# Optimization experiments

Measured on AMD Instinct MI355X. Metric: run time of the kernel, lower is better.

Reference implementation:

```python
import jax, jax.numpy as jnp
import numpy as np

VOCAB = 50000
D = 256          # mem_emb_size == embedding_size (forced by o_q + u)
E = 256
H = E // 2       # LSTM hidden
HOPS = 3
N_MEM, MEM_WORDS = 2000, 50
BATCH, Q_LEN = 64, 50
N_CHOICE, CH_LEN = 4, 10


def setup_inputs() -> dict:
    key = jax.random.key(0)
    ks = jax.random.split(key, 12)
    emb_scale = 0.02
    proj_scale = 1.0 / np.sqrt(E)
    return {
        "memory": jax.random.randint(ks[0], (N_MEM, MEM_WORDS), 0, VOCAB),
        "ques": jax.random.randint(ks[1], (BATCH, Q_LEN), 0, VOCAB),
        "answerChoices": jax.random.randint(ks[2], (BATCH, N_CHOICE, CH_LEN), 0, VOCAB),
        "A_emb": jax.random.normal(ks[3], (HOPS, VOCAB, D), jnp.float32) * emb_scale,
        "B_emb": jax.random.normal(ks[4], (VOCAB, E), jnp.float32) * emb_scale,
        "C_emb": jax.random.normal(ks[5], (VOCAB, E), jnp.float32) * emb_scale,
        "U": jax.random.normal(ks[6], (D, E), jnp.float32) * proj_scale,
        "V": jax.random.normal(ks[7], (D, E), jnp.float32) * proj_scale,
        "W": jax.random.normal(ks[8], (D, D), jnp.float32) * proj_scale,
        "W_ih": jax.random.normal(ks[9], (4 * H, E), jnp.float32) * proj_scale,
        "W_hh": jax.random.normal(ks[10], (4 * H, H), jnp.float32) * (1.0 / np.sqrt(H)),
        "b_ih": jnp.zeros((4 * H,), jnp.float32),
        "b_hh": jnp.zeros((4 * H,), jnp.float32),
    }


def _lstm_final(x, W_ih, W_hh, b_ih, b_hh):
    # x: [B, T, E]; returns concat(h_T, c_T): [B, 2H] (torch gate order i,f,g,o)
    B = x.shape[0]
    Hh = W_hh.shape[1]
    b = b_ih + b_hh

    def step(carry, xt):
        h, c = carry
        g = xt @ W_ih.T + h @ W_hh.T + b
        i, f, gg, o = jnp.split(g, 4, axis=-1)
        c = jax.nn.sigmoid(f) * c + jax.nn.sigmoid(i) * jnp.tanh(gg)
        h = jax.nn.sigmoid(o) * jnp.tanh(c)
        return (h, c), None

    init = (jnp.zeros((B, Hh), x.dtype), jnp.zeros((B, Hh), x.dtype))
    (h, c), _ = jax.lax.scan(step, init, jnp.swapaxes(x, 0, 1))
    return jnp.concatenate([h, c], axis=-1)


def reference(memory, ques, answerChoices, A_emb, B_emb, C_emb, U, V, W,
              W_ih, W_hh, b_ih, b_hh):
    # question encoding: embed -> LSTM -> concat(h, c)   [B, E]
    u = _lstm_final(B_emb[ques], W_ih, W_hh, b_ih, b_hh)
    # answer choices: embedding-bag sum over words       [B, K, E]
    a = C_emb[answerChoices].sum(axis=2)

    hops = A_emb.shape[0]
    o_q = None
    o_a = None
    for hop in range(hops):
        # per-hop memory embedding (shared across batch): gather + sum  [N, D]
        M = A_emb[hop][memory].sum(axis=1)
        # question-side attention over memory slots
        p_q = jax.nn.softmax(jnp.einsum('nd,de,be->bn', M, U, u), axis=1)
        o_q = p_q @ M                      # [B, D]
        u = o_q + u
        # answer-side attention (all choices at once)
        p_a = jax.nn.softmax(jnp.einsum('nd,de,bke->bkn', M, V, a), axis=-1)
        o_a = jnp.einsum('bkn,nd->bkd', p_a, M)   # [B, K, D]
        a = o_a + a

    # prediction: o_q^T W o_a per choice  -> [B, K]
    pred = jnp.einsum('bd,dm,bkm->bk', o_q, W, o_a)
    return jax.nn.log_softmax(pred, axis=1)
```

## Files before the change

### kernel.cpp

```cpp
#include <hip/hip_runtime.h>
#include <hip/hip_bf16.h>
#include <math.h>

#define VOCAB 50000
#define DDIM 256
#define EDIM 256
#define HDIM 128
#define N_MEM 2000
#define MEM_WORDS 50
#define BATCH 64
#define Q_LEN 50
#define N_CHOICE 4
#define CH_LEN 10
#define NT 5
#define BT (BATCH * NT)

__device__ __forceinline__ float sigmoidf_(float x) {
    return 1.0f / (1.0f + expf(-x));
}

__global__ __launch_bounds__(256) void transpose_kernel(const float* __restrict__ in,
                                                        float* __restrict__ out,
                                                        int R, int C) {
    __shared__ float tile[32][33];
    int c0 = blockIdx.x * 32, r0 = blockIdx.y * 32;
    int tx = threadIdx.x & 31, ty = threadIdx.x >> 5;
    for (int i = ty; i < 32; i += 8) {
        int r = r0 + i, c = c0 + tx;
        tile[i][tx] = (r < R && c < C) ? in[(size_t)r * C + c] : 0.0f;
    }
    __syncthreads();
    for (int i = ty; i < 32; i += 8) {
        int r = c0 + i, c = r0 + tx;
        if (r < C && c < R) out[(size_t)r * R + c] = tile[tx][i];
    }
}

__global__ __launch_bounds__(256) void compute_M_kernel(const int* __restrict__ memory,
                                                        const float* __restrict__ A_emb,
                                                        float* __restrict__ M_all) {
    int n = blockIdx.x, hop = blockIdx.y, d = threadIdx.x;
    __shared__ int idx[MEM_WORDS];
    if (d < MEM_WORDS) idx[d] = memory[n * MEM_WORDS + d];
    __syncthreads();
    const float* base = A_emb + (size_t)hop * VOCAB * DDIM;
    float acc = 0.0f;
#pragma unroll 5
    for (int w = 0; w < MEM_WORDS; ++w) acc += base[(size_t)idx[w] * DDIM + d];
    M_all[((size_t)hop * N_MEM + n) * DDIM + d] = acc;
}

__global__ __launch_bounds__(256) void answer_bag_kernel(const int* __restrict__ ach,
                                                         const float* __restrict__ C_emb,
                                                         float* __restrict__ a) {
    int k = blockIdx.x, b = blockIdx.y, d = threadIdx.x;
    __shared__ int idx[CH_LEN];
    if (d < CH_LEN) idx[d] = ach[(b * N_CHOICE + k) * CH_LEN + d];
    __syncthreads();
    float acc = 0.0f;
#pragma unroll
    for (int w = 0; w < CH_LEN; ++w) acc += C_emb[(size_t)idx[w] * EDIM + d];
    a[(size_t)(b * N_CHOICE + k) * EDIM + d] = acc;
}

template <bool GATHER, bool BIAS>
__global__ __launch_bounds__(256) void gemm_abT_kernel(
    const float* __restrict__ A, const float* __restrict__ B, float* __restrict__ C,
    int M, int N, int K, const int* __restrict__ gidx,
    const float* __restrict__ bias1, const float* __restrict__ bias2) {
    __shared__ float As[16][64];
    __shared__ float Bs[16][64];
    __shared__ int rows[64];
    const int tid = threadIdx.x;
    const int m0 = blockIdx.x * 64;
    const int n0 = blockIdx.y * 64;
    const int lrow = tid >> 2;
    const int lk = (tid & 3) << 2;
    const int tx = tid & 15;
    const int ty = tid >> 4;
    if (GATHER) {
        if (tid < 64) rows[tid] = gidx[m0 + tid];
        __syncthreads();
    }
    float acc[4][4] = {};
    for (int k0 = 0; k0 < K; k0 += 16) {
        const float* ap = GATHER ? (A + (size_t)rows[lrow] * K)
                                 : (A + (size_t)(m0 + lrow) * K);
        float4 av = *(const float4*)(ap + k0 + lk);
        float4 bv = make_float4(0.f, 0.f, 0.f, 0.f);
        int brow = n0 + lrow;
        if (brow < N) bv = *(const float4*)(B + (size_t)brow * K + k0 + lk);
        __syncthreads();
        As[lk + 0][lrow] = av.x; As[lk + 1][lrow] = av.y;
        As[lk + 2][lrow] = av.z; As[lk + 3][lrow] = av.w;
        Bs[lk + 0][lrow] = bv.x; Bs[lk + 1][lrow] = bv.y;
        Bs[lk + 2][lrow] = bv.z; Bs[lk + 3][lrow] = bv.w;
        __syncthreads();
#pragma unroll
        for (int kk = 0; kk < 16; ++kk) {
            float4 a4 = *(const float4*)&As[kk][ty * 4];
            float4 b4 = *(const float4*)&Bs[kk][tx * 4];
            acc[0][0] += a4.x * b4.x; acc[0][1] += a4.x * b4.y; acc[0][2] += a4.x * b4.z; acc[0][3] += a4.x * b4.w;
            acc[1][0] += a4.y * b4.x; acc[1][1] += a4.y * b4.y; acc[1][2] += a4.y * b4.z; acc[1][3] += a4.y * b4.w;
            acc[2][0] += a4.z * b4.x; acc[2][1] += a4.z * b4.y; acc[2][2] += a4.z * b4.z; acc[2][3] += a4.z * b4.w;
            acc[3][0] += a4.w * b4.x; acc[3][1] += a4.w * b4.y; acc[3][2] += a4.w * b4.z; acc[3][3] += a4.w * b4.w;
        }
    }
#pragma unroll
    for (int i = 0; i < 4; ++i) {
        int m = m0 + ty * 4 + i;
#pragma unroll
        for (int j = 0; j < 4; ++j) {
            int n = n0 + tx * 4 + j;
            if (n < N) {
                float v = acc[i][j];
                if (BIAS) v += bias1[n] + bias2[n];
                C[(size_t)m * N + n] = v;
            }
        }
    }
}

__global__ __launch_bounds__(256) void gemm_ab_splitk_kernel(
    const float* __restrict__ A, const float* __restrict__ B, float* __restrict__ Cpart,
    int M, int N, int K, int KC) {
    __shared__ float As[16][64];
    __shared__ float Bs[16][64];
    const int tid = threadIdx.x;
    const int m0 = blockIdx.x * 64;
    const int n0 = blockIdx.y * 64;
    const int kstart = blockIdx.z * KC;
    const int kend = min(K, kstart + KC);
    const int arow = tid >> 2;
    const int alk = (tid & 3) << 2;
    const int bk = tid >> 4;
    const int bn = (tid & 15) << 2;
    const int tx = tid & 15;
    const int ty = tid >> 4;
    float acc[4][4] = {};
    for (int k0 = kstart; k0 < kend; k0 += 16) {
        float4 av = *(const float4*)(A + (size_t)(m0 + arow) * K + k0 + alk);
        float4 bv = *(const float4*)(B + (size_t)(k0 + bk) * N + n0 + bn);
        __syncthreads();
        As[alk + 0][arow] = av.x; As[alk + 1][arow] = av.y;
        As[alk + 2][arow] = av.z; As[alk + 3][arow] = av.w;
        *(float4*)&Bs[bk][bn] = bv;
        __syncthreads();
#pragma unroll
        for (int kk = 0; kk < 16; ++kk) {
            float4 a4 = *(const float4*)&As[kk][ty * 4];
            float4 b4 = *(const float4*)&Bs[kk][tx * 4];
            acc[0][0] += a4.x * b4.x; acc[0][1] += a4.x * b4.y; acc[0][2] += a4.x * b4.z; acc[0][3] += a4.x * b4.w;
            acc[1][0] += a4.y * b4.x; acc[1][1] += a4.y * b4.y; acc[1][2] += a4.y * b4.z; acc[1][3] += a4.y * b4.w;
            acc[2][0] += a4.z * b4.x; acc[2][1] += a4.z * b4.y; acc[2][2] += a4.z * b4.z; acc[2][3] += a4.z * b4.w;
            acc[3][0] += a4.w * b4.x; acc[3][1] += a4.w * b4.y; acc[3][2] += a4.w * b4.z; acc[3][3] += a4.w * b4.w;
        }
    }
    float* Cz = Cpart + (size_t)blockIdx.z * M * N;
#pragma unroll
    for (int i = 0; i < 4; ++i)
#pragma unroll
        for (int j = 0; j < 4; ++j)
            Cz[(size_t)(m0 + ty * 4 + i) * N + n0 + tx * 4 + j] = acc[i][j];
}

__global__ __launch_bounds__(512, 2) void lstm_kernel(const float* __restrict__ G0,
                                                      const float* __restrict__ WhhT,
                                                      float* __restrict__ u) {
    const int b = blockIdx.x;
    const int j = threadIdx.x;
    float w[HDIM];
#pragma unroll
    for (int h = 0; h < HDIM; ++h) w[h] = WhhT[(size_t)h * (4 * HDIM) + j];
    __shared__ float sh[HDIM];
    __shared__ float sg[4 * HDIM];
    float c = 0.0f;
    if (j < HDIM) sh[j] = 0.0f;
    __syncthreads();
    const float* g0p = G0 + (size_t)b * Q_LEN * (4 * HDIM) + j;
    for (int t = 0; t < Q_LEN; ++t) {
        float a0 = g0p[(size_t)t * (4 * HDIM)], a1 = 0.f, a2 = 0.f, a3 = 0.f;
#pragma unroll
        for (int h = 0; h < HDIM; h += 4) {
            float4 hv = *(const float4*)&sh[h];
            a0 += w[h + 0] * hv.x;
            a1 += w[h + 1] * hv.y;
            a2 += w[h + 2] * hv.z;
            a3 += w[h + 3] * hv.w;
        }
        sg[j] = (a0 + a1) + (a2 + a3);
        __syncthreads();
        if (j < HDIM) {
            float gi = sg[j], gf = sg[HDIM + j], gg = sg[2 * HDIM + j], go = sg[3 * HDIM + j];
            c = sigmoidf_(gf) * c + sigmoidf_(gi) * tanhf(gg);
            sh[j] = sigmoidf_(go) * tanhf(c);
        }
        __syncthreads();
    }
    if (j < HDIM) {
        u[(size_t)b * EDIM + j] = sh[j];
        u[(size_t)b * EDIM + HDIM + j] = c;
    }
}

__global__ __launch_bounds__(256) void proj_T_kernel(const float* __restrict__ u,
                                                     const float* __restrict__ a,
                                                     const float* __restrict__ UT,
                                                     const float* __restrict__ VT,
                                                     float* __restrict__ T) {
    const int tgt = blockIdx.x;
    const int b = blockIdx.y;
    const int d = threadIdx.x;
    __shared__ float sx[EDIM];
    const float* src = (tgt == 0) ? (u + (size_t)b * EDIM)
                                  : (a + (size_t)(b * N_CHOICE + tgt - 1) * EDIM);
    sx[d] = src[d];
    __syncthreads();
    const float* Wt = (tgt == 0) ? UT : VT;
    float acc = 0.0f;
#pragma unroll 4
    for (int e = 0; e < EDIM; ++e) acc += Wt[(size_t)e * DDIM + d] * sx[e];
    T[(size_t)(b * NT + tgt) * DDIM + d] = acc;
}

__global__ __launch_bounds__(256) void softmax_rows_kernel(float* __restrict__ S, int N) {
    const int row = blockIdx.x;
    float* x = S + (size_t)row * N;
    __shared__ float red[256];
    const int tid = threadIdx.x;
    float mx = -INFINITY;
    for (int i = tid; i < N; i += 256) mx = fmaxf(mx, x[i]);
    red[tid] = mx;
    __syncthreads();
    for (int s = 128; s > 0; s >>= 1) {
        if (tid < s) red[tid] = fmaxf(red[tid], red[tid + s]);
        __syncthreads();
    }
    mx = red[0];
    __syncthreads();
    float sum = 0.0f;
    for (int i = tid; i < N; i += 256) {
        float e = expf(x[i] - mx);
        x[i] = e;
        sum += e;
    }
    red[tid] = sum;
    __syncthreads();
    for (int s = 128; s > 0; s >>= 1) {
        if (tid < s) red[tid] += red[tid + s];
        __syncthreads();
    }
    float inv = 1.0f / red[0];
    for (int i = tid; i < N; i += 256) x[i] *= inv;
}

__global__ __launch_bounds__(256) void reduce_update_kernel(const float* __restrict__ Opart,
                                                            float* __restrict__ O,
                                                            float* __restrict__ u,
                                                            float* __restrict__ a) {
    const int bt = blockIdx.x;
    const int d = threadIdx.x;
    const size_t idx = (size_t)bt * DDIM + d;
    const size_t stride = (size_t)BT * DDIM;
    float v = Opart[idx] + Opart[stride + idx] + Opart[2 * stride + idx] + Opart[3 * stride + idx];
    O[idx] = v;
    const int b = bt / NT, t = bt % NT;
    if (t == 0) u[(size_t)b * EDIM + d] += v;
    else a[(size_t)(b * N_CHOICE + t - 1) * EDIM + d] += v;
}

__global__ __launch_bounds__(256) void predict_kernel(const float* __restrict__ O,
                                                      const float* __restrict__ W,
                                                      float* __restrict__ out) {
    const int b = blockIdx.x;
    const int m = threadIdx.x;
    __shared__ float soq[DDIM];
    __shared__ float red[256];
    __shared__ float scv[N_CHOICE];
    soq[m] = O[(size_t)(b * NT) * DDIM + m];
    __syncthreads();
    float wq = 0.0f;
#pragma unroll 4
    for (int d = 0; d < DDIM; ++d) wq += W[(size_t)d * DDIM + m] * soq[d];
    for (int k = 0; k < N_CHOICE; ++k) {
        red[m] = wq * O[(size_t)(b * NT + 1 + k) * DDIM + m];
        __syncthreads();
        for (int s = 128; s > 0; s >>= 1) {
            if (m < s) red[m] += red[m + s];
            __syncthreads();
        }
        if (m == 0) scv[k] = red[0];
        __syncthreads();
    }
    if (m == 0) {
        float mx = fmaxf(fmaxf(scv[0], scv[1]), fmaxf(scv[2], scv[3]));
        float s = 0.0f;
        for (int k = 0; k < N_CHOICE; ++k) s += expf(scv[k] - mx);
        float ls = mx + logf(s);
        for (int k = 0; k < N_CHOICE; ++k) out[b * N_CHOICE + k] = scv[k] - ls;
    }
}

extern "C" void kernel_launch(void* const* d_in, const int* in_sizes, int n_in,
                              void* d_out, int out_size, void* d_ws, size_t ws_size,
                              hipStream_t stream) {
    const int* memory = (const int*)d_in[0];
    const int* ques = (const int*)d_in[1];
    const int* ach = (const int*)d_in[2];
    const float* A_emb = (const float*)d_in[3];
    const float* B_emb = (const float*)d_in[4];
    const float* C_emb = (const float*)d_in[5];
    const float* U = (const float*)d_in[6];
    const float* V = (const float*)d_in[7];
    const float* W = (const float*)d_in[8];
    const float* W_ih = (const float*)d_in[9];
    const float* W_hh = (const float*)d_in[10];
    const float* b_ih = (const float*)d_in[11];
    const float* b_hh = (const float*)d_in[12];
    float* out = (float*)d_out;

    float* ws = (float*)d_ws;
    float* M_all = ws;
    float* G0 = M_all + 3 * N_MEM * DDIM;
    float* u = G0 + (size_t)BATCH * Q_LEN * 4 * HDIM;
    float* a = u + BATCH * EDIM;
    float* UT = a + BATCH * N_CHOICE * EDIM;
    float* VT = UT + EDIM * DDIM;
    float* WhhT = VT + EDIM * DDIM;
    float* T = G0;
    float* S = T + BT * DDIM;
    float* Opart = S + (size_t)BT * N_MEM;
    float* O = Opart + 4 * (size_t)BT * DDIM;

    transpose_kernel<<<dim3(8, 8), 256, 0, stream>>>(U, UT, DDIM, EDIM);
    transpose_kernel<<<dim3(8, 8), 256, 0, stream>>>(V, VT, DDIM, EDIM);
    transpose_kernel<<<dim3(4, 16), 256, 0, stream>>>(W_hh, WhhT, 4 * HDIM, HDIM);

    compute_M_kernel<<<dim3(N_MEM, 3), 256, 0, stream>>>(memory, A_emb, M_all);

    gemm_abT_kernel<true, true><<<dim3(50, 8), 256, 0, stream>>>(
        B_emb, W_ih, G0, BATCH * Q_LEN, 4 * HDIM, EDIM, ques, b_ih, b_hh);

    lstm_kernel<<<BATCH, 512, 0, stream>>>(G0, WhhT, u);

    answer_bag_kernel<<<dim3(N_CHOICE, BATCH), 256, 0, stream>>>(ach, C_emb, a);

    for (int hop = 0; hop < 3; ++hop) {
        const float* Mh = M_all + (size_t)hop * N_MEM * DDIM;
        proj_T_kernel<<<dim3(NT, BATCH), 256, 0, stream>>>(u, a, UT, VT, T);
        gemm_abT_kernel<false, false><<<dim3(5, 32), 256, 0, stream>>>(
            T, Mh, S, BT, N_MEM, DDIM, nullptr, nullptr, nullptr);
        softmax_rows_kernel<<<BT, 256, 0, stream>>>(S, N_MEM);
        gemm_ab_splitk_kernel<<<dim3(5, 4, 4), 256, 0, stream>>>(
            S, Mh, Opart, BT, DDIM, N_MEM, 512);
        reduce_update_kernel<<<BT, 256, 0, stream>>>(Opart, O, u, a);
    }

    predict_kernel<<<BATCH, 256, 0, stream>>>(O, W, out);
}
```

Before: 654.5 us.

## Vectorize memory gather, shrink GEMM tiles, deepen split-K, defer softmax normalization

The memory-embedding gather now reads float4 values, with four memory slots per block. The GEMM kernels switch to 32x64 tiles with 128 threads, which doubles the block count to better fill the GPU. The split-K for the attention-weighted sum goes from 4 to 10 chunks. Softmax normalization moves into the reduce step: it divides by the row sums there, saving one pass over S. In exchange there are more partial buffers to reduce and the extra workspace layout for the sums must be right.

```diff
diff --git a/kernel.cpp b/kernel.cpp
--- a/kernel.cpp
+++ b/kernel.cpp
@@ -14,6 +14,8 @@
 #define CH_LEN 10
 #define NT 5
 #define BT (BATCH * NT)
+#define OZ 10
+#define OKC 208
 
 __device__ __forceinline__ float sigmoidf_(float x) {
     return 1.0f / (1.0f + expf(-x));
@@ -39,15 +41,22 @@
 __global__ __launch_bounds__(256) void compute_M_kernel(const int* __restrict__ memory,
                                                         const float* __restrict__ A_emb,
                                                         float* __restrict__ M_all) {
-    int n = blockIdx.x, hop = blockIdx.y, d = threadIdx.x;
-    __shared__ int idx[MEM_WORDS];
-    if (d < MEM_WORDS) idx[d] = memory[n * MEM_WORDS + d];
-    __syncthreads();
-    const float* base = A_emb + (size_t)hop * VOCAB * DDIM;
-    float acc = 0.0f;
-#pragma unroll 5
-    for (int w = 0; w < MEM_WORDS; ++w) acc += base[(size_t)idx[w] * DDIM + d];
-    M_all[((size_t)hop * N_MEM + n) * DDIM + d] = acc;
+    const int hop = blockIdx.y;
+    const int tid = threadIdx.x;
+    const int slot = tid >> 6;
+    const int lane = tid & 63;
+    const int n = blockIdx.x * 4 + slot;
+    __shared__ int sidx[4 * MEM_WORDS];
+    if (tid < 4 * MEM_WORDS) sidx[tid] = memory[blockIdx.x * 4 * MEM_WORDS + tid];
+    __syncthreads();
+    const float* base = A_emb + (size_t)hop * VOCAB * DDIM + (lane << 2);
+    float4 acc = make_float4(0.f, 0.f, 0.f, 0.f);
+#pragma unroll 10
+    for (int w = 0; w < MEM_WORDS; ++w) {
+        float4 v = *(const float4*)(base + (size_t)sidx[slot * MEM_WORDS + w] * DDIM);
+        acc.x += v.x; acc.y += v.y; acc.z += v.z; acc.w += v.w;
+    }
+    *(float4*)&M_all[((size_t)hop * N_MEM + n) * DDIM + (lane << 2)] = acc;
 }
 
 __global__ __launch_bounds__(256) void answer_bag_kernel(const int* __restrict__ ach,
@@ -64,37 +73,41 @@
 }
 
 template <bool GATHER, bool BIAS>
-__global__ __launch_bounds__(256) void gemm_abT_kernel(
+__global__ __launch_bounds__(128) void gemm32_abT_kernel(
     const float* __restrict__ A, const float* __restrict__ B, float* __restrict__ C,
     int M, int N, int K, const int* __restrict__ gidx,
     const float* __restrict__ bias1, const float* __restrict__ bias2) {
-    __shared__ float As[16][64];
-    __shared__ float Bs[16][64];
-    __shared__ int rows[64];
+    __shared__ float As[16][36];
+    __shared__ float Bs[16][68];
+    __shared__ int rows[32];
     const int tid = threadIdx.x;
-    const int m0 = blockIdx.x * 64;
+    const int m0 = blockIdx.x * 32;
     const int n0 = blockIdx.y * 64;
-    const int lrow = tid >> 2;
-    const int lk = (tid & 3) << 2;
+    const int arow = tid >> 2;
+    const int ak4 = (tid & 3) << 2;
     const int tx = tid & 15;
     const int ty = tid >> 4;
     if (GATHER) {
-        if (tid < 64) rows[tid] = gidx[m0 + tid];
+        if (tid < 32) rows[tid] = gidx[m0 + tid];
         __syncthreads();
     }
     float acc[4][4] = {};
     for (int k0 = 0; k0 < K; k0 += 16) {
-        const float* ap = GATHER ? (A + (size_t)rows[lrow] * K)
-                                 : (A + (size_t)(m0 + lrow) * K);
-        float4 av = *(const float4*)(ap + k0 + lk);
-        float4 bv = make_float4(0.f, 0.f, 0.f, 0.f);
-        int brow = n0 + lrow;
-        if (brow < N) bv = *(const float4*)(B + (size_t)brow * K + k0 + lk);
-        __syncthreads();
-        As[lk + 0][lrow] = av.x; As[lk + 1][lrow] = av.y;
-        As[lk + 2][lrow] = av.z; As[lk + 3][lrow] = av.w;
-        Bs[lk + 0][lrow] = bv.x; Bs[lk + 1][lrow] = bv.y;
-        Bs[lk + 2][lrow] = bv.z; Bs[lk + 3][lrow] = bv.w;
+        const float* ap = GATHER ? (A + (size_t)rows[arow] * K)
+                                 : (A + (size_t)(m0 + arow) * K);
+        float4 av = *(const float4*)(ap + k0 + ak4);
+        float4 bv0 = make_float4(0.f, 0.f, 0.f, 0.f);
+        float4 bv1 = make_float4(0.f, 0.f, 0.f, 0.f);
+        int br0 = n0 + arow, br1 = n0 + 32 + arow;
+        if (br0 < N) bv0 = *(const float4*)(B + (size_t)br0 * K + k0 + ak4);
+        if (br1 < N) bv1 = *(const float4*)(B + (size_t)br1 * K + k0 + ak4);
+        __syncthreads();
+        As[ak4 + 0][arow] = av.x; As[ak4 + 1][arow] = av.y;
+        As[ak4 + 2][arow] = av.z; As[ak4 + 3][arow] = av.w;
+        Bs[ak4 + 0][arow] = bv0.x; Bs[ak4 + 1][arow] = bv0.y;
+        Bs[ak4 + 2][arow] = bv0.z; Bs[ak4 + 3][arow] = bv0.w;
+        Bs[ak4 + 0][32 + arow] = bv1.x; Bs[ak4 + 1][32 + arow] = bv1.y;
+        Bs[ak4 + 2][32 + arow] = bv1.z; Bs[ak4 + 3][32 + arow] = bv1.w;
         __syncthreads();
 #pragma unroll
         for (int kk = 0; kk < 16; ++kk) {
@@ -121,30 +134,32 @@
     }
 }
 
-__global__ __launch_bounds__(256) void gemm_ab_splitk_kernel(
+__global__ __launch_bounds__(128) void gemm32_ab_splitk_kernel(
     const float* __restrict__ A, const float* __restrict__ B, float* __restrict__ Cpart,
     int M, int N, int K, int KC) {
-    __shared__ float As[16][64];
-    __shared__ float Bs[16][64];
+    __shared__ float As[16][36];
+    __shared__ float Bs[16][68];
     const int tid = threadIdx.x;
-    const int m0 = blockIdx.x * 64;
+    const int m0 = blockIdx.x * 32;
     const int n0 = blockIdx.y * 64;
     const int kstart = blockIdx.z * KC;
     const int kend = min(K, kstart + KC);
     const int arow = tid >> 2;
-    const int alk = (tid & 3) << 2;
+    const int ak4 = (tid & 3) << 2;
     const int bk = tid >> 4;
     const int bn = (tid & 15) << 2;
     const int tx = tid & 15;
     const int ty = tid >> 4;
     float acc[4][4] = {};
     for (int k0 = kstart; k0 < kend; k0 += 16) {
-        float4 av = *(const float4*)(A + (size_t)(m0 + arow) * K + k0 + alk);
-        float4 bv = *(const float4*)(B + (size_t)(k0 + bk) * N + n0 + bn);
-        __syncthreads();
-        As[alk + 0][arow] = av.x; As[alk + 1][arow] = av.y;
-        As[alk + 2][arow] = av.z; As[alk + 3][arow] = av.w;
-        *(float4*)&Bs[bk][bn] = bv;
+        float4 av = *(const float4*)(A + (size_t)(m0 + arow) * K + k0 + ak4);
+        float4 bv0 = *(const float4*)(B + (size_t)(k0 + bk) * N + n0 + bn);
+        float4 bv1 = *(const float4*)(B + (size_t)(k0 + bk + 8) * N + n0 + bn);
+        __syncthreads();
+        As[ak4 + 0][arow] = av.x; As[ak4 + 1][arow] = av.y;
+        As[ak4 + 2][arow] = av.z; As[ak4 + 3][arow] = av.w;
+        *(float4*)&Bs[bk][bn] = bv0;
+        *(float4*)&Bs[bk + 8][bn] = bv1;
         __syncthreads();
 #pragma unroll
         for (int kk = 0; kk < 16; ++kk) {
@@ -223,7 +238,8 @@
     T[(size_t)(b * NT + tgt) * DDIM + d] = acc;
 }
 
-__global__ __launch_bounds__(256) void softmax_rows_kernel(float* __restrict__ S, int N) {
+__global__ __launch_bounds__(256) void softmax_rows_kernel(float* __restrict__ S,
+                                                           float* __restrict__ sums, int N) {
     const int row = blockIdx.x;
     float* x = S + (size_t)row * N;
     __shared__ float red[256];
@@ -250,11 +266,11 @@
         if (tid < s) red[tid] += red[tid + s];
         __syncthreads();
     }
-    float inv = 1.0f / red[0];
-    for (int i = tid; i < N; i += 256) x[i] *= inv;
+    if (tid == 0) sums[row] = red[0];
 }
 
 __global__ __launch_bounds__(256) void reduce_update_kernel(const float* __restrict__ Opart,
+                                                            const float* __restrict__ sums,
                                                             float* __restrict__ O,
                                                             float* __restrict__ u,
                                                             float* __restrict__ a) {
@@ -262,7 +278,10 @@
     const int d = threadIdx.x;
     const size_t idx = (size_t)bt * DDIM + d;
     const size_t stride = (size_t)BT * DDIM;
-    float v = Opart[idx] + Opart[stride + idx] + Opart[2 * stride + idx] + Opart[3 * stride + idx];
+    float v = 0.0f;
+#pragma unroll
+    for (int z = 0; z < OZ; ++z) v += Opart[z * stride + idx];
+    v /= sums[bt];
     O[idx] = v;
     const int b = bt / NT, t = bt % NT;
     if (t == 0) u[(size_t)b * EDIM + d] += v;
@@ -329,16 +348,17 @@
     float* WhhT = VT + EDIM * DDIM;
     float* T = G0;
     float* S = T + BT * DDIM;
-    float* Opart = S + (size_t)BT * N_MEM;
-    float* O = Opart + 4 * (size_t)BT * DDIM;
+    float* sums = S + (size_t)BT * N_MEM;
+    float* Opart = sums + BT;
+    float* O = Opart + (size_t)OZ * BT * DDIM;
 
     transpose_kernel<<<dim3(8, 8), 256, 0, stream>>>(U, UT, DDIM, EDIM);
     transpose_kernel<<<dim3(8, 8), 256, 0, stream>>>(V, VT, DDIM, EDIM);
     transpose_kernel<<<dim3(4, 16), 256, 0, stream>>>(W_hh, WhhT, 4 * HDIM, HDIM);
 
-    compute_M_kernel<<<dim3(N_MEM, 3), 256, 0, stream>>>(memory, A_emb, M_all);
-
-    gemm_abT_kernel<true, true><<<dim3(50, 8), 256, 0, stream>>>(
+    compute_M_kernel<<<dim3(N_MEM / 4, 3), 256, 0, stream>>>(memory, A_emb, M_all);
+
+    gemm32_abT_kernel<true, true><<<dim3(100, 8), 128, 0, stream>>>(
         B_emb, W_ih, G0, BATCH * Q_LEN, 4 * HDIM, EDIM, ques, b_ih, b_hh);
 
     lstm_kernel<<<BATCH, 512, 0, stream>>>(G0, WhhT, u);
@@ -348,12 +368,12 @@
     for (int hop = 0; hop < 3; ++hop) {
         const float* Mh = M_all + (size_t)hop * N_MEM * DDIM;
         proj_T_kernel<<<dim3(NT, BATCH), 256, 0, stream>>>(u, a, UT, VT, T);
-        gemm_abT_kernel<false, false><<<dim3(5, 32), 256, 0, stream>>>(
+        gemm32_abT_kernel<false, false><<<dim3(10, 32), 128, 0, stream>>>(
             T, Mh, S, BT, N_MEM, DDIM, nullptr, nullptr, nullptr);
-        softmax_rows_kernel<<<BT, 256, 0, stream>>>(S, N_MEM);
-        gemm_ab_splitk_kernel<<<dim3(5, 4, 4), 256, 0, stream>>>(
-            S, Mh, Opart, BT, DDIM, N_MEM, 512);
-        reduce_update_kernel<<<BT, 256, 0, stream>>>(Opart, O, u, a);
+        softmax_rows_kernel<<<BT, 256, 0, stream>>>(S, sums, N_MEM);
+        gemm32_ab_splitk_kernel<<<dim3(10, 4, OZ), 128, 0, stream>>>(
+            S, Mh, Opart, BT, DDIM, N_MEM, OKC);
+        reduce_update_kernel<<<BT, 256, 0, stream>>>(Opart, sums, O, u, a);
     }
 
     predict_kernel<<<BATCH, 256, 0, stream>>>(O, W, out);
```

Measured after the change: 613.1 us. 6.3% less time.
